# Performance work log

Hardware: AMD Instinct MI355X
Metric: run time of the kernel (lower is better)

## Reference

```python
import jax, jax.numpy as jnp
import numpy as np
import math

C = 256
K = 64
STAGE_NUM = 3
UNFOLD_SIZES = (1, 3, 5)


def _l2norm(t, axis):
    return t / (1e-6 + jnp.linalg.norm(t, axis=axis, keepdims=True))


def setup_inputs() -> dict:
    key = jax.random.key(0)
    k0, k1, k2 = jax.random.split(key, 3)
    b, h, w = 4, 64, 64
    x = jax.random.normal(k0, (b, C, h, w), dtype=jnp.float32)
    mu0 = jax.random.normal(k1, (1, C, K), dtype=jnp.float32) * math.sqrt(2.0 / K)
    mu0 = _l2norm(mu0, axis=1)  # matches buffer init: normal_(0, sqrt(2/k)) then l2norm over c
    w_scalar = jnp.array(1.0, dtype=jnp.float32)
    # convcat: Conv2d(3c, c, 1); init std = sqrt(2 / (1*1*out_channels)) = sqrt(2/c)
    w_cat = jax.random.normal(k2, (C, 3 * C), dtype=jnp.float32) * math.sqrt(2.0 / C)
    b_cat = jnp.zeros((C,), dtype=jnp.float32)
    return {"x": x, "mu0": mu0, "w": w_scalar, "w_cat": w_cat, "b_cat": b_cat}


def _mwi_forward(x, mu0, w, w_cat, b_cat):
    b, c, h, wd = x.shape
    k = mu0.shape[2]
    mu = jnp.broadcast_to(mu0, (b, c, k))
    feats = []
    for s in UNFOLD_SIZES:
        p = (s - 1) // 2
        xp = jnp.pad(x, ((0, 0), (0, 0), (p, p), (p, p)))
        # im2col: (b, c, s*s, h, w), kernel positions row-major -> matches torch F.unfold then view(b,c,-1)
        patches = jnp.stack([xp[:, :, i:i + h, j:j + wd] for i in range(s) for j in range(s)], axis=2)
        ux = patches.reshape(b, c, s * s * h * wd)  # (b, c, N)
        z = None
        for _ in range(STAGE_NUM):  # EM iterations (no_grad in original)
            z = jax.nn.softmax(jnp.einsum('bcn,bck->bnk', ux, mu), axis=2)  # E-step
            z_ = z / (1e-6 + z.sum(axis=1, keepdims=True))
            mu = _l2norm(jnp.einsum('bcn,bnk->bck', ux, z_), axis=1)  # M-step
        mu = jax.lax.stop_gradient(mu)
        z = jax.lax.stop_gradient(z)
        zf = jnp.einsum('bck,bnk->bcn', mu, z)  # reconstruction (b, c, N)
        zf = zf.reshape(b, c, s, s, h, wd)
        # col2im (F.fold): overlap-add of kernel positions
        out = jnp.zeros((b, c, h + 2 * p, wd + 2 * p), dtype=x.dtype)
        for i in range(s):
            for j in range(s):
                out = out.at[:, :, i:i + h, j:j + wd].add(zf[:, :, i, j])
        feats.append(out[:, :, p:p + h, p:p + wd])
    cat = jnp.concatenate(feats, axis=1)  # (b, 3c, h, w)
    u = jnp.einsum('bihw,oi->bohw', cat, w_cat) + b_cat[None, :, None, None]
    out = jax.nn.relu(u * w + x)
    return out, mu


def reference(x, mu0, w, w_cat, b_cat):
    return _mwi_forward(x, mu0, w, w_cat, b_cat)
```

## Files before the change

kernel.cpp:

```cpp
#include <hip/hip_runtime.h>

typedef float f32x4 __attribute__((ext_vector_type(4)));
typedef short bf16x8 __attribute__((ext_vector_type(8)));
typedef unsigned short u16;
typedef u16 u16x8 __attribute__((ext_vector_type(8)));

#define B 4
#define C 256
#define K 64
#define NN 4096
#define W3C 768
#define CP 264

__device__ __forceinline__ u16 bf_hi(float f) {
    unsigned u = __float_as_uint(f);
    u += 0x7FFFu + ((u >> 16) & 1u);
    return (u16)(u >> 16);
}
__device__ __forceinline__ float bf_f(u16 s) { return __uint_as_float(((unsigned)s) << 16); }

__global__ void k_prep8(const float* __restrict__ src, u16* __restrict__ h,
                        u16* __restrict__ l, int n8) {
    int i = blockIdx.x * 256 + threadIdx.x;
    if (i >= n8) return;
    const float4* s4 = (const float4*)(src + (size_t)i * 8);
    float4 a = s4[0], bb = s4[1];
    float v[8] = {a.x, a.y, a.z, a.w, bb.x, bb.y, bb.z, bb.w};
    u16x8 hv, lv;
    #pragma unroll
    for (int j = 0; j < 8; j++) {
        u16 hh = bf_hi(v[j]);
        hv[j] = hh;
        lv[j] = bf_hi(v[j] - bf_f(hh));
    }
    *(u16x8*)(h + (size_t)i * 8) = hv;
    *(u16x8*)(l + (size_t)i * 8) = lv;
}

__global__ void k_prep_t(const float* __restrict__ x, u16* __restrict__ th,
                         u16* __restrict__ tl) {
    __shared__ float tile[32][33];
    int b = blockIdx.z, c0 = blockIdx.y * 32, n0 = blockIdx.x * 32;
    int tx = threadIdx.x, ty = threadIdx.y;
    #pragma unroll
    for (int j = 0; j < 4; j++)
        tile[ty + j * 8][tx] = x[((size_t)(b * C + c0 + ty + j * 8)) * NN + n0 + tx];
    __syncthreads();
    #pragma unroll
    for (int j = 0; j < 4; j++) {
        int n = n0 + ty + j * 8;
        float v = tile[tx][ty + j * 8];
        u16 hh = bf_hi(v);
        size_t o = ((size_t)(b * NN + n)) * C + c0 + tx;
        th[o] = hh;
        tl[o] = bf_hi(v - bf_f(hh));
    }
}

__global__ void k_initmu(const float* __restrict__ mu0, u16* __restrict__ mh,
                         u16* __restrict__ ml) {
    int k = blockIdx.x, b = blockIdx.y, c = threadIdx.x;
    float v = mu0[c * K + k];
    u16 hh = bf_hi(v);
    size_t o = ((size_t)(b * K + k)) * C + c;
    mh[o] = hh;
    ml[o] = bf_hi(v - bf_f(hh));
}

__global__ __launch_bounds__(256) void k_estep(
        const u16* __restrict__ xth, const u16* __restrict__ xtl,
        const u16* __restrict__ mh_g, const u16* __restrict__ ml_g,
        u16* __restrict__ sh_g, u16* __restrict__ sl_g,
        float* __restrict__ dpart, int p) {
    extern __shared__ char smem[];
    u16* sxh = (u16*)smem;
    u16* sxl = sxh + 64 * CP;
    u16* smh = sxl + 64 * CP;
    u16* sml = smh + 64 * CP;
    float* dred = (float*)(sml + 64 * CP);

    int b = blockIdx.y, ch = blockIdx.x;
    int n0 = ch * 64;
    int tid = threadIdx.x;
    size_t xbase = ((size_t)(b * NN + n0)) * C;
    size_t mbase = ((size_t)(b * K)) * C;
    for (int t = tid; t < 2048; t += 256) {
        int r = t >> 5, cof = (t & 31) * 8;
        *(u16x8*)&sxh[r * CP + cof] = *(const u16x8*)&xth[xbase + (size_t)r * C + cof];
        *(u16x8*)&sxl[r * CP + cof] = *(const u16x8*)&xtl[xbase + (size_t)r * C + cof];
        *(u16x8*)&smh[r * CP + cof] = *(const u16x8*)&mh_g[mbase + (size_t)r * C + cof];
        *(u16x8*)&sml[r * CP + cof] = *(const u16x8*)&ml_g[mbase + (size_t)r * C + cof];
    }
    __syncthreads();

    int w = tid >> 6, l = tid & 63, lg = l >> 4, lr = l & 15;
    f32x4 z4 = {0.f, 0.f, 0.f, 0.f};
    f32x4 acc[4] = {z4, z4, z4, z4};
    for (int cc = 0; cc < 8; cc++) {
        int co = cc * 32 + lg * 8;
        bf16x8 Ah = *(bf16x8*)&sxh[(w * 16 + lr) * CP + co];
        bf16x8 Al = *(bf16x8*)&sxl[(w * 16 + lr) * CP + co];
        #pragma unroll
        for (int kt = 0; kt < 4; kt++) {
            bf16x8 Bh = *(bf16x8*)&smh[(kt * 16 + lr) * CP + co];
            bf16x8 Bl = *(bf16x8*)&sml[(kt * 16 + lr) * CP + co];
            acc[kt] = __builtin_amdgcn_mfma_f32_16x16x32_bf16(Ah, Bh, acc[kt], 0, 0, 0);
            acc[kt] = __builtin_amdgcn_mfma_f32_16x16x32_bf16(Al, Bh, acc[kt], 0, 0, 0);
            acc[kt] = __builtin_amdgcn_mfma_f32_16x16x32_bf16(Ah, Bl, acc[kt], 0, 0, 0);
        }
    }

    float psum[4] = {0.f, 0.f, 0.f, 0.f};
    #pragma unroll
    for (int jj = 0; jj < 4; jj++) {
        int n = n0 + w * 16 + lg * 4 + jj;
        float v0 = acc[0][jj], v1 = acc[1][jj], v2 = acc[2][jj], v3 = acc[3][jj];
        float m = fmaxf(fmaxf(v0, v1), fmaxf(v2, v3));
        #pragma unroll
        for (int off = 1; off <= 8; off <<= 1) m = fmaxf(m, __shfl_xor(m, off));
        float e0 = __expf(v0 - m), e1 = __expf(v1 - m), e2 = __expf(v2 - m), e3 = __expf(v3 - m);
        float s = e0 + e1 + e2 + e3;
        #pragma unroll
        for (int off = 1; off <= 8; off <<= 1) s += __shfl_xor(s, off);
        int y = n >> 6, xx = n & 63;
        float cnt = (float)((min(p, y) + min(p, 63 - y) + 1) * (min(p, xx) + min(p, 63 - xx) + 1));
        float sc = cnt / s;
        float sw[4] = {e0 * sc, e1 * sc, e2 * sc, e3 * sc};
        size_t gb = ((size_t)(b * NN + n)) * K + lr;
        #pragma unroll
        for (int kt = 0; kt < 4; kt++) {
            u16 hh = bf_hi(sw[kt]);
            sh_g[gb + kt * 16] = hh;
            sl_g[gb + kt * 16] = bf_hi(sw[kt] - bf_f(hh));
            psum[kt] += sw[kt];
        }
    }
    #pragma unroll
    for (int kt = 0; kt < 4; kt++)
        dred[(kt * 16 + lr) * 17 + w * 4 + lg] = psum[kt];
    __syncthreads();
    if (tid < 64) {
        float s = 0.f;
        #pragma unroll
        for (int g = 0; g < 16; g++) s += dred[tid * 17 + g];
        dpart[((size_t)(b * 64 + ch)) * K + tid] = s;
    }
}

__global__ __launch_bounds__(256) void k_mstep(
        const u16* __restrict__ xch, const u16* __restrict__ xcl,
        const u16* __restrict__ sh_g, const u16* __restrict__ sl_g,
        float* __restrict__ tpart) {
    extern __shared__ char smem[];
    u16* ssh = (u16*)smem;
    u16* ssl = ssh + 64 * CP;
    u16* sxh = ssl + 64 * CP;
    u16* sxl = sxh + 64 * CP;
    int ct = blockIdx.x, ch = blockIdx.y, b = blockIdx.z;
    int nb = ch * 256, cb = ct * 64;
    int tid = threadIdx.x;
    for (int t = tid; t < 2048; t += 256) {
        int nl = t >> 3, kc = (t & 7) * 8;
        u16x8 vh = *(const u16x8*)&sh_g[((size_t)(b * NN + nb + nl)) * K + kc];
        u16x8 vl = *(const u16x8*)&sl_g[((size_t)(b * NN + nb + nl)) * K + kc];
        #pragma unroll
        for (int j = 0; j < 8; j++) {
            ssh[(kc + j) * CP + nl] = vh[j];
            ssl[(kc + j) * CP + nl] = vl[j];
        }
    }
    for (int t = tid; t < 2048; t += 256) {
        int r = t >> 5, nof = (t & 31) * 8;
        *(u16x8*)&sxh[r * CP + nof] = *(const u16x8*)&xch[((size_t)(b * C + cb + r)) * NN + nb + nof];
        *(u16x8*)&sxl[r * CP + nof] = *(const u16x8*)&xcl[((size_t)(b * C + cb + r)) * NN + nb + nof];
    }
    __syncthreads();

    int w = tid >> 6, l = tid & 63, lg = l >> 4, lr = l & 15;
    f32x4 z4 = {0.f, 0.f, 0.f, 0.f};
    f32x4 acc[4] = {z4, z4, z4, z4};
    for (int nn = 0; nn < 8; nn++) {
        int no = nn * 32 + lg * 8;
        bf16x8 Ah = *(bf16x8*)&ssh[(w * 16 + lr) * CP + no];
        bf16x8 Al = *(bf16x8*)&ssl[(w * 16 + lr) * CP + no];
        #pragma unroll
        for (int ci = 0; ci < 4; ci++) {
            bf16x8 Bh = *(bf16x8*)&sxh[(ci * 16 + lr) * CP + no];
            bf16x8 Bl = *(bf16x8*)&sxl[(ci * 16 + lr) * CP + no];
            acc[ci] = __builtin_amdgcn_mfma_f32_16x16x32_bf16(Ah, Bh, acc[ci], 0, 0, 0);
            acc[ci] = __builtin_amdgcn_mfma_f32_16x16x32_bf16(Al, Bh, acc[ci], 0, 0, 0);
            acc[ci] = __builtin_amdgcn_mfma_f32_16x16x32_bf16(Ah, Bl, acc[ci], 0, 0, 0);
        }
    }
    #pragma unroll
    for (int ci = 0; ci < 4; ci++)
        #pragma unroll
        for (int jj = 0; jj < 4; jj++) {
            int k = w * 16 + lg * 4 + jj;
            tpart[((size_t)((b * 16 + ch) * K + k)) * C + cb + ci * 16 + lr] = acc[ci][jj];
        }
}

__global__ void k_norm(const float* __restrict__ tpart, const float* __restrict__ dpart,
                       u16* __restrict__ mh_g, u16* __restrict__ ml_g,
                       float* __restrict__ muf, float dconst) {
    __shared__ float red[256];
    int k = blockIdx.x, b = blockIdx.y, tid = threadIdx.x;
    float dv = 0.f;
    if (tid < 64) dv = dpart[((size_t)(b * 64 + tid)) * K + k];
    red[tid] = dv; __syncthreads();
    for (int s = 128; s > 0; s >>= 1) { if (tid < s) red[tid] += red[tid + s]; __syncthreads(); }
    float d = dconst + red[0];
    __syncthreads();
    float tt = 0.f;
    #pragma unroll
    for (int chn = 0; chn < 16; chn++)
        tt += tpart[((size_t)((b * 16 + chn) * K + k)) * C + tid];
    red[tid] = tt * tt; __syncthreads();
    for (int s = 128; s > 0; s >>= 1) { if (tid < s) red[tid] += red[tid + s]; __syncthreads(); }
    float inv = 1.f / (1e-6f * d + sqrtf(red[0]));
    float v = tt * inv;
    size_t o = ((size_t)(b * K + k)) * C + tid;
    u16 hh = bf_hi(v);
    mh_g[o] = hh;
    ml_g[o] = bf_hi(v - bf_f(hh));
    muf[((size_t)(b * C + tid)) * K + k] = v;
}

__global__ __launch_bounds__(256) void k_pmat(
        const u16* __restrict__ wch, const u16* __restrict__ wcl,
        const u16* __restrict__ mh_g, const u16* __restrict__ ml_g,
        u16* __restrict__ Pb, int s) {
    int ob = blockIdx.x, b = blockIdx.y;
    int tid = threadIdx.x, w = tid >> 6, l = tid & 63, lg = l >> 4, lr = l & 15;
    f32x4 z4 = {0.f, 0.f, 0.f, 0.f};
    f32x4 acc[4] = {z4, z4, z4, z4};
    int orow = ob * 64 + w * 16 + lr;
    const u16* wbh = wch + (size_t)orow * W3C + s * C;
    const u16* wbl = wcl + (size_t)orow * W3C + s * C;
    for (int cc = 0; cc < 8; cc++) {
        int co = cc * 32 + lg * 8;
        bf16x8 Ah = *(const bf16x8*)&wbh[co];
        bf16x8 Al = *(const bf16x8*)&wbl[co];
        #pragma unroll
        for (int kt = 0; kt < 4; kt++) {
            bf16x8 Bh = *(const bf16x8*)&mh_g[((size_t)(b * K + kt * 16 + lr)) * C + co];
            bf16x8 Bl = *(const bf16x8*)&ml_g[((size_t)(b * K + kt * 16 + lr)) * C + co];
            acc[kt] = __builtin_amdgcn_mfma_f32_16x16x32_bf16(Ah, Bh, acc[kt], 0, 0, 0);
            acc[kt] = __builtin_amdgcn_mfma_f32_16x16x32_bf16(Al, Bh, acc[kt], 0, 0, 0);
            acc[kt] = __builtin_amdgcn_mfma_f32_16x16x32_bf16(Ah, Bl, acc[kt], 0, 0, 0);
        }
    }
    #pragma unroll
    for (int kt = 0; kt < 4; kt++)
        #pragma unroll
        for (int jj = 0; jj < 4; jj++) {
            int o = ob * 64 + w * 16 + lg * 4 + jj;
            Pb[((size_t)((s * B + b) * C + o)) * K + kt * 16 + lr] = bf_hi(acc[kt][jj]);
        }
}

__global__ __launch_bounds__(256) void k_final(
        const u16* __restrict__ sh_g, const u16* __restrict__ Pb,
        const float* __restrict__ x, const float* __restrict__ b_cat,
        const float* __restrict__ wscal, float* __restrict__ out) {
    __shared__ u16 ssig[64 * 72];
    __shared__ u16 sP[64 * 72];
    __shared__ float tbuf[64 * 68];
    int nt = blockIdx.x, ot = blockIdx.y, b = blockIdx.z;
    int n0 = nt * 64, o0 = ot * 64;
    int tid = threadIdx.x, w = tid >> 6, l = tid & 63, lg = l >> 4, lr = l & 15;
    f32x4 z4 = {0.f, 0.f, 0.f, 0.f};
    f32x4 acc[4] = {z4, z4, z4, z4};
    for (int s = 0; s < 3; s++) {
        __syncthreads();
        for (int t = tid; t < 512; t += 256) {
            int r = t >> 3, kc = (t & 7) * 8;
            *(u16x8*)&ssig[r * 72 + kc] =
                *(const u16x8*)&sh_g[(size_t)s * ((size_t)B * NN * K) + ((size_t)(b * NN + n0 + r)) * K + kc];
            *(u16x8*)&sP[r * 72 + kc] =
                *(const u16x8*)&Pb[((size_t)((s * B + b) * C + o0 + r)) * K + kc];
        }
        __syncthreads();
        #pragma unroll
        for (int kk = 0; kk < 2; kk++) {
            int ko = kk * 32 + lg * 8;
            bf16x8 A = *(bf16x8*)&ssig[(w * 16 + lr) * 72 + ko];
            #pragma unroll
            for (int oi = 0; oi < 4; oi++) {
                bf16x8 Bv = *(bf16x8*)&sP[(oi * 16 + lr) * 72 + ko];
                acc[oi] = __builtin_amdgcn_mfma_f32_16x16x32_bf16(A, Bv, acc[oi], 0, 0, 0);
            }
        }
    }
    __syncthreads();
    #pragma unroll
    for (int oi = 0; oi < 4; oi++)
        #pragma unroll
        for (int jj = 0; jj < 4; jj++)
            tbuf[(oi * 16 + lr) * 68 + (w * 16 + lg * 4 + jj)] = acc[oi][jj];
    __syncthreads();
    float wv = wscal[0];
    for (int t = tid; t < 1024; t += 256) {
        int ol = t >> 4, ck = (t & 15) * 4;
        int o = o0 + ol;
        float bc = b_cat[o];
        float4 u4 = *(float4*)&tbuf[ol * 68 + ck];
        size_t base = ((size_t)(b * C + o)) * NN + n0 + ck;
        float4 xv = *(const float4*)&x[base];
        float4 r;
        r.x = fmaxf((u4.x + bc) * wv + xv.x, 0.f);
        r.y = fmaxf((u4.y + bc) * wv + xv.y, 0.f);
        r.z = fmaxf((u4.z + bc) * wv + xv.z, 0.f);
        r.w = fmaxf((u4.w + bc) * wv + xv.w, 0.f);
        *(float4*)&out[base] = r;
    }
}

extern "C" void kernel_launch(void* const* d_in, const int* in_sizes, int n_in,
                              void* d_out, int out_size, void* d_ws, size_t ws_size,
                              hipStream_t stream) {
    const float* x     = (const float*)d_in[0];
    const float* mu0   = (const float*)d_in[1];
    const float* wsc   = (const float*)d_in[2];
    const float* w_cat = (const float*)d_in[3];
    const float* b_cat = (const float*)d_in[4];
    float* out = (float*)d_out;
    char* wsb = (char*)d_ws;

    const size_t SZ_XT = (size_t)B * NN * C * 2;
    u16* xth  = (u16*)(wsb);
    u16* xtl  = (u16*)(wsb + SZ_XT);
    u16* xch  = (u16*)(wsb + 2 * SZ_XT);
    u16* xcl  = (u16*)(wsb + 3 * SZ_XT);
    u16* muth = (u16*)(wsb + 4 * SZ_XT);
    u16* mutl = (u16*)(wsb + 4 * SZ_XT + 131072);
    u16* sigh = (u16*)(wsb + 4 * SZ_XT + 262144);
    u16* sigl = (u16*)(wsb + 4 * SZ_XT + 262144 + 6291456);
    float* tpart = (float*)(wsb + 4 * SZ_XT + 262144 + 8388608);
    float* dpart = (float*)((char*)tpart + 4194304);
    u16*   Pb    = (u16*)((char*)dpart + 65536);
    float* muf   = (float*)((char*)Pb + 393216);
    u16*   wch   = (u16*)((char*)muf + 262144);
    u16*   wcl   = wch + (size_t)C * W3C;

    const int ESTEP_LDS = 4 * 64 * CP * 2 + 64 * 17 * 4;
    const int MSTEP_LDS = 4 * 64 * CP * 2;
    hipFuncSetAttribute((const void*)k_estep, hipFuncAttributeMaxDynamicSharedMemorySize, ESTEP_LDS);
    hipFuncSetAttribute((const void*)k_mstep, hipFuncAttributeMaxDynamicSharedMemorySize, MSTEP_LDS);

    k_prep8<<<2048, 256, 0, stream>>>(x, xch, xcl, B * C * NN / 8);
    k_prep_t<<<dim3(128, 8, B), dim3(32, 8), 0, stream>>>(x, xth, xtl);
    k_prep8<<<96, 256, 0, stream>>>(w_cat, wch, wcl, C * W3C / 8);
    k_initmu<<<dim3(K, B), 256, 0, stream>>>(mu0, muth, mutl);

    const int   pvals[3]   = {0, 1, 2};
    const float dconsts[3] = {1e-6f, 1e-6f + 764.f / 64.f, 1e-6f + 3804.f / 64.f};

    for (int s = 0; s < 3; s++) {
        u16* shs = sigh + (size_t)s * B * NN * K;
        for (int it = 0; it < 3; it++) {
            k_estep<<<dim3(64, B), 256, ESTEP_LDS, stream>>>(xth, xtl, muth, mutl,
                                                             shs, sigl, dpart, pvals[s]);
            k_mstep<<<dim3(4, 16, B), 256, MSTEP_LDS, stream>>>(xch, xcl, shs, sigl, tpart);
            k_norm<<<dim3(K, B), 256, 0, stream>>>(tpart, dpart, muth, mutl, muf, dconsts[s]);
        }
        k_pmat<<<dim3(4, B), 256, 0, stream>>>(wch, wcl, muth, mutl, Pb, s);
    }
    k_final<<<dim3(64, 4, B), 256, 0, stream>>>(sigh, Pb, x, b_cat, wsc, out);
    hipMemcpyAsync(out + (size_t)B * C * NN, muf, (size_t)B * C * K * sizeof(float),
                   hipMemcpyDeviceToDevice, stream);
}
```

Baseline: 283.8 us.

## Fuse E-step and M-step into one kernel and drop transposed x copy

Result: slower. 316.2 us (+11.4%).

```diff
diff --git a/kernel.cpp b/kernel.cpp
--- a/kernel.cpp
+++ b/kernel.cpp
@@ -4,6 +4,7 @@
 typedef short bf16x8 __attribute__((ext_vector_type(8)));
 typedef unsigned short u16;
 typedef u16 u16x8 __attribute__((ext_vector_type(8)));
+typedef unsigned int u32;
 
 #define B 4
 #define C 256
@@ -11,6 +12,7 @@
 #define NN 4096
 #define W3C 768
 #define CP 264
+#define SP 72
 
 __device__ __forceinline__ u16 bf_hi(float f) {
     unsigned u = __float_as_uint(f);
@@ -19,87 +21,94 @@
 }
 __device__ __forceinline__ float bf_f(u16 s) { return __uint_as_float(((unsigned)s) << 16); }
 
-__global__ void k_prep8(const float* __restrict__ src, u16* __restrict__ h,
-                        u16* __restrict__ l, int n8) {
-    int i = blockIdx.x * 256 + threadIdx.x;
-    if (i >= n8) return;
-    const float4* s4 = (const float4*)(src + (size_t)i * 8);
-    float4 a = s4[0], bb = s4[1];
-    float v[8] = {a.x, a.y, a.z, a.w, bb.x, bb.y, bb.z, bb.w};
-    u16x8 hv, lv;
-    #pragma unroll
-    for (int j = 0; j < 8; j++) {
-        u16 hh = bf_hi(v[j]);
-        hv[j] = hh;
-        lv[j] = bf_hi(v[j] - bf_f(hh));
-    }
-    *(u16x8*)(h + (size_t)i * 8) = hv;
-    *(u16x8*)(l + (size_t)i * 8) = lv;
-}
-
-__global__ void k_prep_t(const float* __restrict__ x, u16* __restrict__ th,
-                         u16* __restrict__ tl) {
-    __shared__ float tile[32][33];
-    int b = blockIdx.z, c0 = blockIdx.y * 32, n0 = blockIdx.x * 32;
-    int tx = threadIdx.x, ty = threadIdx.y;
-    #pragma unroll
-    for (int j = 0; j < 4; j++)
-        tile[ty + j * 8][tx] = x[((size_t)(b * C + c0 + ty + j * 8)) * NN + n0 + tx];
-    __syncthreads();
-    #pragma unroll
-    for (int j = 0; j < 4; j++) {
-        int n = n0 + ty + j * 8;
-        float v = tile[tx][ty + j * 8];
+__global__ void k_prep(const float* __restrict__ x, const float* __restrict__ mu0,
+                       const float* __restrict__ w_cat,
+                       u16* __restrict__ xch, u16* __restrict__ xcl,
+                       u16* __restrict__ wch, u16* __restrict__ wcl,
+                       u16* __restrict__ muth, u16* __restrict__ mutl) {
+    int blk = blockIdx.x, tid = threadIdx.x;
+    if (blk < 2048) {
+        int i = blk * 256 + tid;
+        const float4* s4 = (const float4*)(x + (size_t)i * 8);
+        float4 a = s4[0], bq = s4[1];
+        float v[8] = {a.x, a.y, a.z, a.w, bq.x, bq.y, bq.z, bq.w};
+        u16x8 hv, lv;
+        #pragma unroll
+        for (int j = 0; j < 8; j++) { u16 hh = bf_hi(v[j]); hv[j] = hh; lv[j] = bf_hi(v[j] - bf_f(hh)); }
+        *(u16x8*)(xch + (size_t)i * 8) = hv;
+        *(u16x8*)(xcl + (size_t)i * 8) = lv;
+    } else if (blk < 2144) {
+        int i = (blk - 2048) * 256 + tid;
+        const float4* s4 = (const float4*)(w_cat + (size_t)i * 8);
+        float4 a = s4[0], bq = s4[1];
+        float v[8] = {a.x, a.y, a.z, a.w, bq.x, bq.y, bq.z, bq.w};
+        u16x8 hv, lv;
+        #pragma unroll
+        for (int j = 0; j < 8; j++) { u16 hh = bf_hi(v[j]); hv[j] = hh; lv[j] = bf_hi(v[j] - bf_f(hh)); }
+        *(u16x8*)(wch + (size_t)i * 8) = hv;
+        *(u16x8*)(wcl + (size_t)i * 8) = lv;
+    } else {
+        int g = (blk - 2144) * 256 + tid;
+        int kq = (g >> 8) & 63, cq = g & 255;
+        float v = mu0[cq * K + kq];
         u16 hh = bf_hi(v);
-        size_t o = ((size_t)(b * NN + n)) * C + c0 + tx;
-        th[o] = hh;
-        tl[o] = bf_hi(v - bf_f(hh));
-    }
-}
-
-__global__ void k_initmu(const float* __restrict__ mu0, u16* __restrict__ mh,
-                         u16* __restrict__ ml) {
-    int k = blockIdx.x, b = blockIdx.y, c = threadIdx.x;
-    float v = mu0[c * K + k];
-    u16 hh = bf_hi(v);
-    size_t o = ((size_t)(b * K + k)) * C + c;
-    mh[o] = hh;
-    ml[o] = bf_hi(v - bf_f(hh));
-}
-
-__global__ __launch_bounds__(256) void k_estep(
-        const u16* __restrict__ xth, const u16* __restrict__ xtl,
-        const u16* __restrict__ mh_g, const u16* __restrict__ ml_g,
-        u16* __restrict__ sh_g, u16* __restrict__ sl_g,
-        float* __restrict__ dpart, int p) {
+        muth[g] = hh;
+        mutl[g] = bf_hi(v - bf_f(hh));
+    }
+}
+
+__global__ __launch_bounds__(256) void k_em(
+        const u16* __restrict__ xch, const u16* __restrict__ xcl,
+        const u16* __restrict__ muth, const u16* __restrict__ mutl,
+        float* __restrict__ tpart, float* __restrict__ dpart,
+        u16* __restrict__ sig_out, int pv, int write_sig)
+{
     extern __shared__ char smem[];
     u16* sxh = (u16*)smem;
     u16* sxl = sxh + 64 * CP;
     u16* smh = sxl + 64 * CP;
     u16* sml = smh + 64 * CP;
-    float* dred = (float*)(sml + 64 * CP);
-
-    int b = blockIdx.y, ch = blockIdx.x;
-    int n0 = ch * 64;
-    int tid = threadIdx.x;
-    size_t xbase = ((size_t)(b * NN + n0)) * C;
-    size_t mbase = ((size_t)(b * K)) * C;
-    for (int t = tid; t < 2048; t += 256) {
-        int r = t >> 5, cof = (t & 31) * 8;
-        *(u16x8*)&sxh[r * CP + cof] = *(const u16x8*)&xth[xbase + (size_t)r * C + cof];
-        *(u16x8*)&sxl[r * CP + cof] = *(const u16x8*)&xtl[xbase + (size_t)r * C + cof];
-        *(u16x8*)&smh[r * CP + cof] = *(const u16x8*)&mh_g[mbase + (size_t)r * C + cof];
-        *(u16x8*)&sml[r * CP + cof] = *(const u16x8*)&ml_g[mbase + (size_t)r * C + cof];
-    }
-    __syncthreads();
-
-    int w = tid >> 6, l = tid & 63, lg = l >> 4, lr = l & 15;
+    u16* sTh = sml + 64 * CP;
+    u16* sTl = sTh + 64 * SP;
+    float* redf = (float*)(sTl + 64 * SP);
+
+    const int ch = blockIdx.x, b = blockIdx.y, tid = threadIdx.x;
+    const int n0 = ch * 64;
+
+    {
+        int p2 = tid & 127, h = tid >> 7;
+        #pragma unroll
+        for (int nc = 0; nc < 4; nc++) {
+            int nrow = h * 32 + nc * 8;
+            u16x8 a0h = *(const u16x8*)&xch[((size_t)(b * C + 2 * p2)) * NN + n0 + nrow];
+            u16x8 a1h = *(const u16x8*)&xch[((size_t)(b * C + 2 * p2 + 1)) * NN + n0 + nrow];
+            u16x8 a0l = *(const u16x8*)&xcl[((size_t)(b * C + 2 * p2)) * NN + n0 + nrow];
+            u16x8 a1l = *(const u16x8*)&xcl[((size_t)(b * C + 2 * p2 + 1)) * NN + n0 + nrow];
+            #pragma unroll
+            for (int j = 0; j < 8; j++) {
+                *(u32*)&sxh[(nrow + j) * CP + 2 * p2] = (u32)a0h[j] | ((u32)a1h[j] << 16);
+                *(u32*)&sxl[(nrow + j) * CP + 2 * p2] = (u32)a0l[j] | ((u32)a1l[j] << 16);
+            }
+        }
+    }
+    {
+        size_t mbase = ((size_t)(b * K)) * C;
+        for (int t = tid; t < 2048; t += 256) {
+            int r = t >> 5, cof = (t & 31) * 8;
+            *(u16x8*)&smh[r * CP + cof] = *(const u16x8*)&muth[mbase + (size_t)r * C + cof];
+            *(u16x8*)&sml[r * CP + cof] = *(const u16x8*)&mutl[mbase + (size_t)r * C + cof];
+        }
+    }
+    __syncthreads();
+
+    const int wid = tid >> 6, l = tid & 63, lg = l >> 4, lr = l & 15;
     f32x4 z4 = {0.f, 0.f, 0.f, 0.f};
+
     f32x4 acc[4] = {z4, z4, z4, z4};
     for (int cc = 0; cc < 8; cc++) {
         int co = cc * 32 + lg * 8;
-        bf16x8 Ah = *(bf16x8*)&sxh[(w * 16 + lr) * CP + co];
-        bf16x8 Al = *(bf16x8*)&sxl[(w * 16 + lr) * CP + co];
+        bf16x8 Ah = *(bf16x8*)&sxh[(wid * 16 + lr) * CP + co];
+        bf16x8 Al = *(bf16x8*)&sxl[(wid * 16 + lr) * CP + co];
         #pragma unroll
         for (int kt = 0; kt < 4; kt++) {
             bf16x8 Bh = *(bf16x8*)&smh[(kt * 16 + lr) * CP + co];
@@ -110,121 +119,107 @@
         }
     }
 
+    float swv[4][4];
     float psum[4] = {0.f, 0.f, 0.f, 0.f};
     #pragma unroll
     for (int jj = 0; jj < 4; jj++) {
-        int n = n0 + w * 16 + lg * 4 + jj;
+        int n = n0 + wid * 16 + lg * 4 + jj;
         float v0 = acc[0][jj], v1 = acc[1][jj], v2 = acc[2][jj], v3 = acc[3][jj];
         float m = fmaxf(fmaxf(v0, v1), fmaxf(v2, v3));
         #pragma unroll
         for (int off = 1; off <= 8; off <<= 1) m = fmaxf(m, __shfl_xor(m, off));
         float e0 = __expf(v0 - m), e1 = __expf(v1 - m), e2 = __expf(v2 - m), e3 = __expf(v3 - m);
-        float s = e0 + e1 + e2 + e3;
-        #pragma unroll
-        for (int off = 1; off <= 8; off <<= 1) s += __shfl_xor(s, off);
+        float ss = e0 + e1 + e2 + e3;
+        #pragma unroll
+        for (int off = 1; off <= 8; off <<= 1) ss += __shfl_xor(ss, off);
         int y = n >> 6, xx = n & 63;
-        float cnt = (float)((min(p, y) + min(p, 63 - y) + 1) * (min(p, xx) + min(p, 63 - xx) + 1));
-        float sc = cnt / s;
-        float sw[4] = {e0 * sc, e1 * sc, e2 * sc, e3 * sc};
-        size_t gb = ((size_t)(b * NN + n)) * K + lr;
+        float cnt = (float)((min(pv, y) + min(pv, 63 - y) + 1) * (min(pv, xx) + min(pv, 63 - xx) + 1));
+        float sc = cnt / ss;
+        swv[jj][0] = e0 * sc; swv[jj][1] = e1 * sc; swv[jj][2] = e2 * sc; swv[jj][3] = e3 * sc;
         #pragma unroll
         for (int kt = 0; kt < 4; kt++) {
-            u16 hh = bf_hi(sw[kt]);
-            sh_g[gb + kt * 16] = hh;
-            sl_g[gb + kt * 16] = bf_hi(sw[kt] - bf_f(hh));
-            psum[kt] += sw[kt];
-        }
-    }
-    #pragma unroll
-    for (int kt = 0; kt < 4; kt++)
-        dred[(kt * 16 + lr) * 17 + w * 4 + lg] = psum[kt];
+            psum[kt] += swv[jj][kt];
+            if (write_sig)
+                sig_out[((size_t)(b * NN + n)) * K + kt * 16 + lr] = bf_hi(swv[jj][kt]);
+        }
+    }
+    #pragma unroll
+    for (int kt = 0; kt < 4; kt++) {
+        #pragma unroll
+        for (int jp = 0; jp < 2; jp++) {
+            float va = swv[2 * jp][kt], vb = swv[2 * jp + 1][kt];
+            u16 ha = bf_hi(va), hb = bf_hi(vb);
+            u16 la = bf_hi(va - bf_f(ha)), lb = bf_hi(vb - bf_f(hb));
+            int col = wid * 16 + lg * 4 + 2 * jp;
+            *(u32*)&sTh[(kt * 16 + lr) * SP + col] = (u32)ha | ((u32)hb << 16);
+            *(u32*)&sTl[(kt * 16 + lr) * SP + col] = (u32)la | ((u32)lb << 16);
+        }
+        redf[(kt * 16 + lr) * 17 + wid * 4 + lg] = psum[kt];
+    }
     __syncthreads();
     if (tid < 64) {
-        float s = 0.f;
-        #pragma unroll
-        for (int g = 0; g < 16; g++) s += dred[tid * 17 + g];
-        dpart[((size_t)(b * 64 + ch)) * K + tid] = s;
-    }
-}
-
-__global__ __launch_bounds__(256) void k_mstep(
-        const u16* __restrict__ xch, const u16* __restrict__ xcl,
-        const u16* __restrict__ sh_g, const u16* __restrict__ sl_g,
-        float* __restrict__ tpart) {
-    extern __shared__ char smem[];
-    u16* ssh = (u16*)smem;
-    u16* ssl = ssh + 64 * CP;
-    u16* sxh = ssl + 64 * CP;
-    u16* sxl = sxh + 64 * CP;
-    int ct = blockIdx.x, ch = blockIdx.y, b = blockIdx.z;
-    int nb = ch * 256, cb = ct * 64;
-    int tid = threadIdx.x;
-    for (int t = tid; t < 2048; t += 256) {
-        int nl = t >> 3, kc = (t & 7) * 8;
-        u16x8 vh = *(const u16x8*)&sh_g[((size_t)(b * NN + nb + nl)) * K + kc];
-        u16x8 vl = *(const u16x8*)&sl_g[((size_t)(b * NN + nb + nl)) * K + kc];
-        #pragma unroll
-        for (int j = 0; j < 8; j++) {
-            ssh[(kc + j) * CP + nl] = vh[j];
-            ssl[(kc + j) * CP + nl] = vl[j];
-        }
-    }
-    for (int t = tid; t < 2048; t += 256) {
-        int r = t >> 5, nof = (t & 31) * 8;
-        *(u16x8*)&sxh[r * CP + nof] = *(const u16x8*)&xch[((size_t)(b * C + cb + r)) * NN + nb + nof];
-        *(u16x8*)&sxl[r * CP + nof] = *(const u16x8*)&xcl[((size_t)(b * C + cb + r)) * NN + nb + nof];
-    }
-    __syncthreads();
-
-    int w = tid >> 6, l = tid & 63, lg = l >> 4, lr = l & 15;
-    f32x4 z4 = {0.f, 0.f, 0.f, 0.f};
-    f32x4 acc[4] = {z4, z4, z4, z4};
-    for (int nn = 0; nn < 8; nn++) {
-        int no = nn * 32 + lg * 8;
-        bf16x8 Ah = *(bf16x8*)&ssh[(w * 16 + lr) * CP + no];
-        bf16x8 Al = *(bf16x8*)&ssl[(w * 16 + lr) * CP + no];
-        #pragma unroll
-        for (int ci = 0; ci < 4; ci++) {
-            bf16x8 Bh = *(bf16x8*)&sxh[(ci * 16 + lr) * CP + no];
-            bf16x8 Bl = *(bf16x8*)&sxl[(ci * 16 + lr) * CP + no];
-            acc[ci] = __builtin_amdgcn_mfma_f32_16x16x32_bf16(Ah, Bh, acc[ci], 0, 0, 0);
-            acc[ci] = __builtin_amdgcn_mfma_f32_16x16x32_bf16(Al, Bh, acc[ci], 0, 0, 0);
-            acc[ci] = __builtin_amdgcn_mfma_f32_16x16x32_bf16(Ah, Bl, acc[ci], 0, 0, 0);
-        }
-    }
-    #pragma unroll
-    for (int ci = 0; ci < 4; ci++)
-        #pragma unroll
-        for (int jj = 0; jj < 4; jj++) {
-            int k = w * 16 + lg * 4 + jj;
-            tpart[((size_t)((b * 16 + ch) * K + k)) * C + cb + ci * 16 + lr] = acc[ci][jj];
-        }
-}
-
-__global__ void k_norm(const float* __restrict__ tpart, const float* __restrict__ dpart,
-                       u16* __restrict__ mh_g, u16* __restrict__ ml_g,
-                       float* __restrict__ muf, float dconst) {
+        float sd = 0.f;
+        #pragma unroll
+        for (int g2 = 0; g2 < 16; g2++) sd += redf[tid * 17 + g2];
+        dpart[((size_t)(b * 64 + ch)) * K + tid] = sd;
+    }
+
+    f32x4 macc[16];
+    #pragma unroll
+    for (int ci = 0; ci < 16; ci++) macc[ci] = z4;
+    #pragma unroll
+    for (int nn2 = 0; nn2 < 2; nn2++) {
+        int no = nn2 * 32 + lg * 8;
+        bf16x8 Ah = *(bf16x8*)&sTh[(wid * 16 + lr) * SP + no];
+        bf16x8 Al = *(bf16x8*)&sTl[(wid * 16 + lr) * SP + no];
+        #pragma unroll
+        for (int ci = 0; ci < 16; ci++) {
+            size_t go = ((size_t)(b * C + ci * 16 + lr)) * NN + n0 + no;
+            bf16x8 Bh = *(const bf16x8*)&xch[go];
+            bf16x8 Bl = *(const bf16x8*)&xcl[go];
+            macc[ci] = __builtin_amdgcn_mfma_f32_16x16x32_bf16(Ah, Bh, macc[ci], 0, 0, 0);
+            macc[ci] = __builtin_amdgcn_mfma_f32_16x16x32_bf16(Al, Bh, macc[ci], 0, 0, 0);
+            macc[ci] = __builtin_amdgcn_mfma_f32_16x16x32_bf16(Ah, Bl, macc[ci], 0, 0, 0);
+        }
+    }
+    #pragma unroll
+    for (int ci = 0; ci < 16; ci++)
+        #pragma unroll
+        for (int jj = 0; jj < 4; jj++)
+            tpart[((size_t)((b * 64 + ch) * K + wid * 16 + lg * 4 + jj)) * C + ci * 16 + lr]
+                = macc[ci][jj];
+}
+
+__global__ __launch_bounds__(256) void k_norm(
+        const float* __restrict__ tpart, const float* __restrict__ dpart,
+        u16* __restrict__ muth, u16* __restrict__ mutl,
+        float* __restrict__ out_mu, float dconst) {
     __shared__ float red[256];
+    __shared__ float dsh;
     int k = blockIdx.x, b = blockIdx.y, tid = threadIdx.x;
     float dv = 0.f;
     if (tid < 64) dv = dpart[((size_t)(b * 64 + tid)) * K + k];
-    red[tid] = dv; __syncthreads();
-    for (int s = 128; s > 0; s >>= 1) { if (tid < s) red[tid] += red[tid + s]; __syncthreads(); }
-    float d = dconst + red[0];
-    __syncthreads();
+    #pragma unroll
+    for (int off = 1; off <= 32; off <<= 1) dv += __shfl_xor(dv, off);
+    if (tid == 0) dsh = dv;
     float tt = 0.f;
-    #pragma unroll
-    for (int chn = 0; chn < 16; chn++)
-        tt += tpart[((size_t)((b * 16 + chn) * K + k)) * C + tid];
-    red[tid] = tt * tt; __syncthreads();
-    for (int s = 128; s > 0; s >>= 1) { if (tid < s) red[tid] += red[tid + s]; __syncthreads(); }
+    #pragma unroll 8
+    for (int chn = 0; chn < 64; chn++)
+        tt += tpart[((size_t)((b * 64 + chn) * K + k)) * C + tid];
+    red[tid] = tt * tt;
+    __syncthreads();
+    for (int st = 128; st > 0; st >>= 1) {
+        if (tid < st) red[tid] += red[tid + st];
+        __syncthreads();
+    }
+    float d = dconst + dsh;
     float inv = 1.f / (1e-6f * d + sqrtf(red[0]));
     float v = tt * inv;
+    u16 hh = bf_hi(v);
     size_t o = ((size_t)(b * K + k)) * C + tid;
-    u16 hh = bf_hi(v);
-    mh_g[o] = hh;
-    ml_g[o] = bf_hi(v - bf_f(hh));
-    muf[((size_t)(b * C + tid)) * K + k] = v;
+    muth[o] = hh;
+    mutl[o] = bf_hi(v - bf_f(hh));
+    out_mu[((size_t)(b * C + tid)) * K + k] = v;
 }
 
 __global__ __launch_bounds__(256) void k_pmat(
@@ -328,46 +323,45 @@
     float* out = (float*)d_out;
     char* wsb = (char*)d_ws;
 
-    const size_t SZ_XT = (size_t)B * NN * C * 2;
-    u16* xth  = (u16*)(wsb);
-    u16* xtl  = (u16*)(wsb + SZ_XT);
-    u16* xch  = (u16*)(wsb + 2 * SZ_XT);
-    u16* xcl  = (u16*)(wsb + 3 * SZ_XT);
-    u16* muth = (u16*)(wsb + 4 * SZ_XT);
-    u16* mutl = (u16*)(wsb + 4 * SZ_XT + 131072);
-    u16* sigh = (u16*)(wsb + 4 * SZ_XT + 262144);
-    u16* sigl = (u16*)(wsb + 4 * SZ_XT + 262144 + 6291456);
-    float* tpart = (float*)(wsb + 4 * SZ_XT + 262144 + 8388608);
-    float* dpart = (float*)((char*)tpart + 4194304);
-    u16*   Pb    = (u16*)((char*)dpart + 65536);
-    float* muf   = (float*)((char*)Pb + 393216);
-    u16*   wch   = (u16*)((char*)muf + 262144);
-    u16*   wcl   = wch + (size_t)C * W3C;
-
-    const int ESTEP_LDS = 4 * 64 * CP * 2 + 64 * 17 * 4;
-    const int MSTEP_LDS = 4 * 64 * CP * 2;
-    hipFuncSetAttribute((const void*)k_estep, hipFuncAttributeMaxDynamicSharedMemorySize, ESTEP_LDS);
-    hipFuncSetAttribute((const void*)k_mstep, hipFuncAttributeMaxDynamicSharedMemorySize, MSTEP_LDS);
-
-    k_prep8<<<2048, 256, 0, stream>>>(x, xch, xcl, B * C * NN / 8);
-    k_prep_t<<<dim3(128, 8, B), dim3(32, 8), 0, stream>>>(x, xth, xtl);
-    k_prep8<<<96, 256, 0, stream>>>(w_cat, wch, wcl, C * W3C / 8);
-    k_initmu<<<dim3(K, B), 256, 0, stream>>>(mu0, muth, mutl);
+    const size_t SZ_XC   = (size_t)B * C * NN * 2;
+    const size_t SZ_MUT  = (size_t)B * K * C * 2;
+    const size_t SZ_SIGH = (size_t)3 * B * NN * K * 2;
+    const size_t SZ_TP   = (size_t)B * 64 * K * C * 4;
+    const size_t SZ_DP   = (size_t)B * 64 * K * 4;
+    const size_t SZ_PB   = (size_t)3 * B * C * K * 2;
+    const size_t SZ_WC   = (size_t)C * W3C * 2;
+
+    size_t off = 0;
+    u16*   xch  = (u16*)(wsb + off); off += SZ_XC;
+    u16*   xcl  = (u16*)(wsb + off); off += SZ_XC;
+    u16*   muth = (u16*)(wsb + off); off += SZ_MUT;
+    u16*   mutl = (u16*)(wsb + off); off += SZ_MUT;
+    u16*   sigh = (u16*)(wsb + off); off += SZ_SIGH;
+    float* tpart= (float*)(wsb + off); off += SZ_TP;
+    float* dpart= (float*)(wsb + off); off += SZ_DP;
+    u16*   Pb   = (u16*)(wsb + off); off += SZ_PB;
+    u16*   wch  = (u16*)(wsb + off); off += SZ_WC;
+    u16*   wcl  = (u16*)(wsb + off); off += SZ_WC;
+    float* out_mu = out + (size_t)B * C * NN;
+
+    const int EM_LDS = 4 * 64 * CP * 2 + 2 * 64 * SP * 2 + 1088 * 4;
+    hipFuncSetAttribute((const void*)k_em, hipFuncAttributeMaxDynamicSharedMemorySize, EM_LDS);
+
+    k_prep<<<2400, 256, 0, stream>>>(x, mu0, w_cat, xch, xcl, wch, wcl, muth, mutl);
 
     const int   pvals[3]   = {0, 1, 2};
-    const float dconsts[3] = {1e-6f, 1e-6f + 764.f / 64.f, 1e-6f + 3804.f / 64.f};
+    const float dconsts[3] = {1e-6f, 1e-6f + 11.9375f, 1e-6f + 59.4375f};
 
     for (int s = 0; s < 3; s++) {
-        u16* shs = sigh + (size_t)s * B * NN * K;
+        u16* shs = sigh + (size_t)s * ((size_t)B * NN * K);
         for (int it = 0; it < 3; it++) {
-            k_estep<<<dim3(64, B), 256, ESTEP_LDS, stream>>>(xth, xtl, muth, mutl,
-                                                             shs, sigl, dpart, pvals[s]);
-            k_mstep<<<dim3(4, 16, B), 256, MSTEP_LDS, stream>>>(xch, xcl, shs, sigl, tpart);
-            k_norm<<<dim3(K, B), 256, 0, stream>>>(tpart, dpart, muth, mutl, muf, dconsts[s]);
+            k_em<<<dim3(64, B), 256, EM_LDS, stream>>>(xch, xcl, muth, mutl,
+                                                       tpart, dpart, shs, pvals[s],
+                                                       (it == 2) ? 1 : 0);
+            k_norm<<<dim3(K, B), 256, 0, stream>>>(tpart, dpart, muth, mutl,
+                                                   out_mu, dconsts[s]);
         }
         k_pmat<<<dim3(4, B), 256, 0, stream>>>(wch, wcl, muth, mutl, Pb, s);
     }
     k_final<<<dim3(64, 4, B), 256, 0, stream>>>(sigh, Pb, x, b_cat, wsc, out);
-    hipMemcpyAsync(out + (size_t)B * C * NN, muf, (size_t)B * C * K * sizeof(float),
-                   hipMemcpyDeviceToDevice, stream);
-}
+}
```
